# Optimization experiments

Hardware: AMD Instinct MI355X
Metric: run time of the kernel (lower is better)

## Reference

```python
import jax, jax.numpy as jnp
import numpy as np

COMMITMENT_COST = 0.25

def setup_inputs() -> dict:
    key = jax.random.key(0)
    k1, k2 = jax.random.split(key)
    z = jax.random.normal(k1, (32768, 512), dtype=jnp.float32)
    # codebook initialized uniform(-1/K, 1/K) as in the torch module
    K = 8192
    W = jax.random.uniform(k2, (K, 512), dtype=jnp.float32, minval=-1.0 / K, maxval=1.0 / K)
    return {"z": z, "W": W}

def reference(z, W):
    # z: [B, D], W: [K, D]
    # squared-distance expansion: ||z||^2 + ||w||^2 - 2 z.w
    d2 = (jnp.sum(z * z, axis=1, keepdims=True)
          + jnp.sum(W * W, axis=1)
          - 2.0 * jnp.einsum('bd,kd->bk', z, W))  # [B, K]
    indices = jnp.argmin(d2, axis=1)              # [B]
    z_q_raw = W[indices]                          # [B, D]
    e_latent_loss = jnp.mean((jax.lax.stop_gradient(z_q_raw) - z) ** 2)
    q_latent_loss = jnp.mean((z_q_raw - jax.lax.stop_gradient(z)) ** 2)
    vq_loss = q_latent_loss + COMMITMENT_COST * e_latent_loss
    # straight-through estimator
    z_q = z + jax.lax.stop_gradient(z_q_raw - z)
    return (z_q, indices, vq_loss)
```

## Files before the change

kernel.cpp:

```cpp
#include <hip/hip_runtime.h>
#include <stdint.h>


#define B_ROWS 32768
#define DIM    512
#define KCODES 8192
#define SUPERS 4
#define TILES  16
#define ZROWS  64
#define NSTEP  256

typedef short bhalf8_t __attribute__((ext_vector_type(8)));
typedef float f32x4_t  __attribute__((ext_vector_type(4)));

__device__ __forceinline__ float b2f(unsigned short u) {
    return __uint_as_float(((unsigned int)u) << 16);
}
__device__ __forceinline__ unsigned short f2b(float f) {
    unsigned int x = __float_as_uint(f);
    return (unsigned short)((x + 0x7FFFu + ((x >> 16) & 1u)) >> 16);
}
__device__ __forceinline__ void gl_lds16(const void* g, void* l) {
    __builtin_amdgcn_global_load_lds(
        (const __attribute__((address_space(1))) unsigned int*)g,
        (__attribute__((address_space(3))) unsigned int*)l, 16, 0, 0);
}

__global__ __launch_bounds__(256) void k_split(const float4* __restrict__ src,
                                               ushort4* __restrict__ dst, int n4) {
    int i = blockIdx.x * 256 + threadIdx.x;
    int stride = gridDim.x * 256;
    for (; i < n4; i += stride) {
        float4 v = src[i];
        ushort4 h;
        h.x = f2b(v.x); h.y = f2b(v.y); h.z = f2b(v.z); h.w = f2b(v.w);
        dst[i] = h;
    }
}

__global__ __launch_bounds__(256) void k_pairsq(const float* __restrict__ X,
                                                float* __restrict__ out, int nrows) {
    int wid = threadIdx.x >> 6, lane = threadIdx.x & 63;
    int r = blockIdx.x * 4 + wid;
    if (r >= nrows) return;
    int b = lane >> 3, j = lane & 7;
    float acc = 0.f;
    if (b < 4) {
        const float* x = X + (size_t)r * DIM + b * 128 + j;
        float v = x[0];
        acc = __fmul_rn(v, v);
        for (int i = 1; i < 16; i++) {
            float w = x[8 * i];
            acc = __fadd_rn(acc, __fmul_rn(w, w));
        }
    }
    float t = __fadd_rn(acc, __shfl_xor(acc, 1));
    t = __fadd_rn(t, __shfl_xor(t, 2));
    t = __fadd_rn(t, __shfl_xor(t, 4));
    float u = __fadd_rn(t, __shfl_xor(t, 8));
    u = __fadd_rn(u, __shfl_xor(u, 16));
    if (lane == 0) out[r] = u;
}

__device__ __forceinline__ void compute_ks(const unsigned char* zl, int ks,
                                           const unsigned char* wbuf,
                                           int lane, f32x4_t acc[4][2]) {
    bhalf8_t af[4], bf[2];
#pragma unroll
    for (int f = 0; f < 4; f++)
        af[f] = *(const bhalf8_t*)(zl + ks * 4096 + f * 1024 + lane * 16);
#pragma unroll
    for (int f = 0; f < 2; f++)
        bf[f] = *(const bhalf8_t*)(wbuf + f * 1024 + lane * 16);
#pragma unroll
    for (int fm = 0; fm < 4; fm++)
#pragma unroll
        for (int fn = 0; fn < 2; fn++)
            acc[fm][fn] = __builtin_amdgcn_mfma_f32_16x16x32_bf16(af[fm], bf[fn], acc[fm][fn], 0, 0, 0);
}

__global__ __launch_bounds__(256) void k_argmin(const unsigned short* __restrict__ Zh,
                                                const unsigned short* __restrict__ Wh,
                                                const float* __restrict__ ww,
                                                float2* __restrict__ part) {
    __shared__ alignas(16) unsigned char smem[81920];
    const int tid = threadIdx.x;
    const int lane = tid & 63, w = tid >> 6;
    const int lane15 = lane & 15, q = lane >> 4;
    const int b = blockIdx.x;
    const int super = b & 3;
    const int rb = (b >> 2) * ZROWS;

    unsigned char* zl  = smem;
    unsigned char* wpr = smem + 65536 + w * 4096;

    {
        const int m = tid & 15;
        const int kseg8 = ((tid >> 4) & 3) << 3;
#pragma unroll
        for (int i = 0; i < 16; i++) {
            const int s = i * 256 + tid;
            const int ks = s >> 8;
            const int g = (s >> 6) & 3;
            gl_lds16(Zh + (size_t)(rb + g * 16 + m) * DIM + ks * 32 + kseg8,
                     zl + s * 16);
        }
    }

    const int colL = lane & 15;
    const int ksegL8 = (q & 3) << 3;
#define STAGE_W(ST, WB)                                                                   \
    do {                                                                                  \
        const int _nt = super * 2048 + ((ST) >> 4) * 128 + w * 32;                        \
        const int _kg = ((ST) & 15) * 32 + ksegL8;                                        \
        gl_lds16(Wh + (size_t)(_nt + colL) * DIM + _kg,      (WB) + lane * 16);           \
        gl_lds16(Wh + (size_t)(_nt + 16 + colL) * DIM + _kg, (WB) + 1024 + lane * 16);    \
    } while (0)

    uint32_t p1[4][4], p2[4][4];
#pragma unroll
    for (int i = 0; i < 4; i++)
#pragma unroll
        for (int jj = 0; jj < 4; jj++) { p1[i][jj] = 0xFFFFFFFFu; p2[i][jj] = 0xFFFFFFFFu; }

    STAGE_W(0, wpr);
    __syncthreads();

    for (int tl = 0; tl < TILES; ++tl) {
        const int nt = super * 2048 + tl * 128;
        float cb[2];
        cb[0] = ww[nt + w * 32 + lane15] + 0.5f;
        cb[1] = ww[nt + w * 32 + 16 + lane15] + 0.5f;

        f32x4_t acc[4][2];
#pragma unroll
        for (int i = 0; i < 4; i++)
#pragma unroll
            for (int jj = 0; jj < 2; jj++) acc[i][jj] = (f32x4_t){0.f, 0.f, 0.f, 0.f};

        for (int k2 = 0; k2 < 16; k2 += 2) {
            const int st = tl * 16 + k2;
            STAGE_W(st + 1, wpr + 2048);
            asm volatile("s_waitcnt vmcnt(2)" ::: "memory");
            compute_ks(zl, k2, wpr, lane, acc);
            if (st + 2 < NSTEP) {
                STAGE_W(st + 2, wpr);
                asm volatile("s_waitcnt vmcnt(2)" ::: "memory");
            } else {
                asm volatile("s_waitcnt vmcnt(0)" ::: "memory");
            }
            compute_ks(zl, k2 + 1, wpr + 2048, lane, acc);
        }

#pragma unroll
        for (int fm = 0; fm < 4; fm++)
#pragma unroll
            for (int r = 0; r < 4; r++)
#pragma unroll
                for (int fn = 0; fn < 2; fn++) {
                    float sv = fmaf(-2.0f, acc[fm][fn][r], cb[fn]);
                    uint32_t pk = (__float_as_uint(sv) & 0xFFFFFF80u) | (uint32_t)(tl * 2 + fn);
                    if (pk < p1[fm][r]) { p2[fm][r] = p1[fm][r]; p1[fm][r] = pk; }
                    else if (pk < p2[fm][r]) { p2[fm][r] = pk; }
                }
    }
#undef STAGE_W

    __syncthreads();
    uint32_t* keys = (uint32_t*)smem;
#pragma unroll
    for (int fm = 0; fm < 4; fm++)
#pragma unroll
        for (int r = 0; r < 4; r++) {
            int row = fm * 16 + q * 4 + r;
            int sp = w * 16 + lane15;
            keys[row * 130 + sp * 2 + 0] = p1[fm][r];
            keys[row * 130 + sp * 2 + 1] = p2[fm][r];
        }
    __syncthreads();
    if (tid < ZROWS) {
        int row = tid;
        int rglob = rb + row;
        for (int s = 0; s < 4; s++) {
            uint32_t bk = 0xFFFFFFFFu; int be = 0;
            for (int e = 0; e < 128; e++) {
                uint32_t k = keys[row * 130 + e];
                if (k < bk) { bk = k; be = e; }
            }
            int sp = be >> 1;
            int id = (int)(bk & 127u);
            int n = super * 2048 + (id >> 1) * 128 + (sp >> 4) * 32 + (id & 1) * 16 + (sp & 15);
            part[((size_t)rglob * SUPERS + super) * 4 + s] =
                make_float2(__uint_as_float(bk), __int_as_float(n));
            keys[row * 130 + be] = 0xFFFFFFFFu;
        }
    }
}

__global__ __launch_bounds__(256) void k_exact(const float* __restrict__ Zf,
                                               const float* __restrict__ Wf,
                                               const float2* __restrict__ part,
                                               const float* __restrict__ zz,
                                               const float* __restrict__ ww,
                                               float* __restrict__ outf,
                                               float* __restrict__ lossp) {
    __shared__ float wsum[4];
    int wid = threadIdx.x >> 6, lane = threadIdx.x & 63;
    int r = blockIdx.x * 4 + wid;
    int c = lane >> 2, j = lane & 3;

    float2 P = part[((size_t)r * SUPERS + (c >> 2)) * 4 + (c & 3)];
    int n = __float_as_int(P.y);
    n = min(max(n, 0), KCODES - 1);

    const float* zp = Zf + (size_t)r * DIM + j;
    const float* wp = Wf + (size_t)n * DIM + j;
    float acc = 0.f;
    for (int i = 0; i < 128; i++)
        acc = __fadd_rn(acc, __fmul_rn(zp[4 * i], wp[4 * i]));
    float t = __fadd_rn(acc, __shfl_xor(acc, 1));
    t = __fadd_rn(t, __shfl_xor(t, 2));
    float dot = __shfl(t, c * 4);

    float t1 = __fadd_rn(zz[r], ww[n]);
    float t2 = __fmul_rn(2.0f, dot);
    float d2 = __fadd_rn(t1, -t2);

    float bd = (j == 0) ? d2 : 3.4e38f;
    int   bn = (j == 0) ? n  : 0x7FFFFFFF;
#pragma unroll
    for (int off = 32; off; off >>= 1) {
        float od = __shfl_xor(bd, off);
        int   on = __shfl_xor(bn, off);
        if (od < bd || (od == bd && on < bn)) { bd = od; bn = on; }
    }
    int idx = bn;

    float4 wa = *(const float4*)(Wf + (size_t)idx * DIM + lane * 8);
    float4 wb = *(const float4*)(Wf + (size_t)idx * DIM + lane * 8 + 4);
    float4 za = *(const float4*)(Zf + (size_t)r   * DIM + lane * 8);
    float4 zb = *(const float4*)(Zf + (size_t)r   * DIM + lane * 8 + 4);
    *(float4*)(outf + (size_t)r * DIM + lane * 8)     = wa;
    *(float4*)(outf + (size_t)r * DIM + lane * 8 + 4) = wb;
    float d0 = za.x - wa.x, d1 = za.y - wa.y, dd2 = za.z - wa.z, d3 = za.w - wa.w;
    float d4 = zb.x - wb.x, d5 = zb.y - wb.y, d6 = zb.z - wb.z, d7 = zb.w - wb.w;
    float ls = d0*d0 + d1*d1 + dd2*dd2 + d3*d3 + d4*d4 + d5*d5 + d6*d6 + d7*d7;
#pragma unroll
    for (int off = 32; off; off >>= 1) ls += __shfl_xor(ls, off);
    if (lane == 0) {
        outf[(size_t)B_ROWS * DIM + r] = (float)idx;
        wsum[wid] = ls;
    }
    __syncthreads();
    if (threadIdx.x == 0) lossp[blockIdx.x] = wsum[0] + wsum[1] + wsum[2] + wsum[3];
}

__global__ __launch_bounds__(256) void k_loss(const float* __restrict__ lossp,
                                              float* __restrict__ outf) {
    __shared__ float sm[256];
    float a = 0.f;
    for (int i = threadIdx.x; i < 8192; i += 256) a += lossp[i];
    sm[threadIdx.x] = a;
    __syncthreads();
    for (int s = 128; s; s >>= 1) {
        if (threadIdx.x < s) sm[threadIdx.x] += sm[threadIdx.x + s];
        __syncthreads();
    }
    if (threadIdx.x == 0)
        outf[(size_t)B_ROWS * DIM + B_ROWS] = 1.25f * sm[0] / 16777216.0f;
}

extern "C" void kernel_launch(void* const* d_in, const int* in_sizes, int n_in,
                              void* d_out, int out_size, void* d_ws, size_t ws_size,
                              hipStream_t stream) {
    (void)in_sizes; (void)n_in; (void)out_size; (void)ws_size;
    const float* Zf = (const float*)d_in[0];
    const float* Wf = (const float*)d_in[1];
    float* outf = (float*)d_out;

    unsigned short* Zh = (unsigned short*)d_out;
    unsigned short* Wh = (unsigned short*)((char*)d_out + (32ull << 20));

    float*  ww    = (float*)d_ws;
    float*  zz    = (float*)((char*)d_ws + 32768);
    float*  lossp = (float*)((char*)d_ws + 163840);
    float2* partp = (float2*)((char*)d_ws + 196608);

    k_split<<<1024, 256, 0, stream>>>((const float4*)Zf, (ushort4*)Zh, B_ROWS * DIM / 4);
    k_split<<<512,  256, 0, stream>>>((const float4*)Wf, (ushort4*)Wh, KCODES * DIM / 4);
    k_pairsq<<<KCODES / 4, 256, 0, stream>>>(Wf, ww, KCODES);
    k_pairsq<<<B_ROWS / 4, 256, 0, stream>>>(Zf, zz, B_ROWS);
    k_argmin<<<(B_ROWS / ZROWS) * SUPERS, 256, 0, stream>>>(Zh, Wh, ww, partp);
    k_exact<<<B_ROWS / 4, 256, 0, stream>>>(Zf, Wf, partp, zz, ww, outf, lossp);
    k_loss<<<1, 256, 0, stream>>>(lossp, outf);
}
```

Before: 793.3 us.

## Load codebook fragments directly into registers with 4-deep prefetch instead of LDS staging

The codebook operand is no longer staged through per-wave LDS buffers with global_load_lds and manual vmcnt waits. Each wave now loads its W fragments straight from global memory into a 4-slot register ring, prefetching 4 k-steps ahead, with the k-loop fully unrolled. This removes the LDS round trip and the 16KB of W staging space, trading it for more VGPRs and reliance on compiler-inserted waits for latency hiding.

After: 945.0 us. 1.19x slower.

```diff
diff --git a/kernel.cpp b/kernel.cpp
--- a/kernel.cpp
+++ b/kernel.cpp
@@ -62,28 +62,34 @@
     if (lane == 0) out[r] = u;
 }
 
-__device__ __forceinline__ void compute_ks(const unsigned char* zl, int ks,
-                                           const unsigned char* wbuf,
-                                           int lane, f32x4_t acc[4][2]) {
-    bhalf8_t af[4], bf[2];
+__device__ __forceinline__ void loadW(const unsigned short* __restrict__ Wh,
+                                      int super, int w, int lane15, int q, int st,
+                                      bhalf8_t& o0, bhalf8_t& o1) {
+    const int nt = super * 2048 + (st >> 4) * 128 + w * 32;
+    const unsigned short* p = Wh + (size_t)(nt + lane15) * DIM + (st & 15) * 32 + q * 8;
+    o0 = *(const bhalf8_t*)(p);
+    o1 = *(const bhalf8_t*)(p + 16 * DIM);
+}
+
+__device__ __forceinline__ void computeA(const unsigned char* zl, int ks, int lane,
+                                         bhalf8_t b0, bhalf8_t b1,
+                                         f32x4_t acc[4][2]) {
+    bhalf8_t af[4];
 #pragma unroll
     for (int f = 0; f < 4; f++)
         af[f] = *(const bhalf8_t*)(zl + ks * 4096 + f * 1024 + lane * 16);
 #pragma unroll
-    for (int f = 0; f < 2; f++)
-        bf[f] = *(const bhalf8_t*)(wbuf + f * 1024 + lane * 16);
-#pragma unroll
-    for (int fm = 0; fm < 4; fm++)
-#pragma unroll
-        for (int fn = 0; fn < 2; fn++)
-            acc[fm][fn] = __builtin_amdgcn_mfma_f32_16x16x32_bf16(af[fm], bf[fn], acc[fm][fn], 0, 0, 0);
+    for (int fm = 0; fm < 4; fm++) {
+        acc[fm][0] = __builtin_amdgcn_mfma_f32_16x16x32_bf16(af[fm], b0, acc[fm][0], 0, 0, 0);
+        acc[fm][1] = __builtin_amdgcn_mfma_f32_16x16x32_bf16(af[fm], b1, acc[fm][1], 0, 0, 0);
+    }
 }
 
 __global__ __launch_bounds__(256) void k_argmin(const unsigned short* __restrict__ Zh,
                                                 const unsigned short* __restrict__ Wh,
                                                 const float* __restrict__ ww,
                                                 float2* __restrict__ part) {
-    __shared__ alignas(16) unsigned char smem[81920];
+    __shared__ alignas(16) unsigned char smem[65536];
     const int tid = threadIdx.x;
     const int lane = tid & 63, w = tid >> 6;
     const int lane15 = lane & 15, q = lane >> 4;
@@ -91,8 +97,7 @@
     const int super = b & 3;
     const int rb = (b >> 2) * ZROWS;
 
-    unsigned char* zl  = smem;
-    unsigned char* wpr = smem + 65536 + w * 4096;
+    unsigned char* zl = smem;
 
     {
         const int m = tid & 15;
@@ -107,30 +112,23 @@
         }
     }
 
-    const int colL = lane & 15;
-    const int ksegL8 = (q & 3) << 3;
-#define STAGE_W(ST, WB)                                                                   \
-    do {                                                                                  \
-        const int _nt = super * 2048 + ((ST) >> 4) * 128 + w * 32;                        \
-        const int _kg = ((ST) & 15) * 32 + ksegL8;                                        \
-        gl_lds16(Wh + (size_t)(_nt + colL) * DIM + _kg,      (WB) + lane * 16);           \
-        gl_lds16(Wh + (size_t)(_nt + 16 + colL) * DIM + _kg, (WB) + 1024 + lane * 16);    \
-    } while (0)
-
     uint32_t p1[4][4], p2[4][4];
 #pragma unroll
     for (int i = 0; i < 4; i++)
 #pragma unroll
         for (int jj = 0; jj < 4; jj++) { p1[i][jj] = 0xFFFFFFFFu; p2[i][jj] = 0xFFFFFFFFu; }
 
-    STAGE_W(0, wpr);
+    bhalf8_t wr[4][2];
+#pragma unroll
+    for (int p = 0; p < 4; p++)
+        loadW(Wh, super, w, lane15, q, p, wr[p][0], wr[p][1]);
+
     __syncthreads();
 
     for (int tl = 0; tl < TILES; ++tl) {
         const int nt = super * 2048 + tl * 128;
-        float cb[2];
-        cb[0] = ww[nt + w * 32 + lane15] + 0.5f;
-        cb[1] = ww[nt + w * 32 + 16 + lane15] + 0.5f;
+        float cb0 = ww[nt + w * 32 + lane15] + 0.5f;
+        float cb1 = ww[nt + w * 32 + 16 + lane15] + 0.5f;
 
         f32x4_t acc[4][2];
 #pragma unroll
@@ -138,18 +136,12 @@
 #pragma unroll
             for (int jj = 0; jj < 2; jj++) acc[i][jj] = (f32x4_t){0.f, 0.f, 0.f, 0.f};
 
-        for (int k2 = 0; k2 < 16; k2 += 2) {
+#pragma unroll
+        for (int k2 = 0; k2 < 16; ++k2) {
             const int st = tl * 16 + k2;
-            STAGE_W(st + 1, wpr + 2048);
-            asm volatile("s_waitcnt vmcnt(2)" ::: "memory");
-            compute_ks(zl, k2, wpr, lane, acc);
-            if (st + 2 < NSTEP) {
-                STAGE_W(st + 2, wpr);
-                asm volatile("s_waitcnt vmcnt(2)" ::: "memory");
-            } else {
-                asm volatile("s_waitcnt vmcnt(0)" ::: "memory");
-            }
-            compute_ks(zl, k2 + 1, wpr + 2048, lane, acc);
+            computeA(zl, k2, lane, wr[k2 & 3][0], wr[k2 & 3][1], acc);
+            if (st + 4 < NSTEP)
+                loadW(Wh, super, w, lane15, q, st + 4, wr[k2 & 3][0], wr[k2 & 3][1]);
         }
 
 #pragma unroll
@@ -158,13 +150,12 @@
             for (int r = 0; r < 4; r++)
 #pragma unroll
                 for (int fn = 0; fn < 2; fn++) {
-                    float sv = fmaf(-2.0f, acc[fm][fn][r], cb[fn]);
+                    float sv = fmaf(-2.0f, acc[fm][fn][r], fn ? cb1 : cb0);
                     uint32_t pk = (__float_as_uint(sv) & 0xFFFFFF80u) | (uint32_t)(tl * 2 + fn);
                     if (pk < p1[fm][r]) { p2[fm][r] = p1[fm][r]; p1[fm][r] = pk; }
                     else if (pk < p2[fm][r]) { p2[fm][r] = pk; }
                 }
     }
-#undef STAGE_W
 
     __syncthreads();
     uint32_t* keys = (uint32_t*)smem;
```
